# Kernel optimization log

Hardware: AMD Instinct MI355X
Metric: run time of the kernel (lower is better)

The kernel has to match this reference:

```python
import jax, jax.numpy as jnp
import numpy as np

P = 1_500_000
N_DEPTH = 6 * 118 * 16 * 44  # 498432 flattened depth bins
N_FEAT = 6 * 16 * 44         # 4224 flattened feature rows
TOTAL_BEV = 40000            # 200x200 BEV grid
C = 80


def setup_inputs() -> dict:
    key = jax.random.key(0)
    k1, k2, k3, k4, k5, k6, k7 = jax.random.split(key, 7)
    depth = jax.random.uniform(k1, (6, 118, 16, 44), dtype=jnp.float32)
    feat = jax.random.normal(k2, (6, 16, 44, C), dtype=jnp.float32)
    ranks_depth = jax.random.randint(k3, (P,), 0, N_DEPTH, dtype=jnp.int64)
    ranks_feat = jax.random.randint(k4, (P,), 0, N_FEAT, dtype=jnp.int64)
    ranks_bev = jnp.sort(jax.random.randint(k5, (P,), 0, TOTAL_BEV, dtype=jnp.int64))
    interval_starts = jnp.sort(jax.random.randint(k6, (TOTAL_BEV,), 0, P, dtype=jnp.int64))
    interval_lengths = jax.random.randint(k7, (TOTAL_BEV,), 0, 64, dtype=jnp.int64)
    return {
        "depth": depth,
        "feat": feat,
        "ranks_depth": ranks_depth,
        "ranks_feat": ranks_feat,
        "ranks_bev": ranks_bev,
        "interval_starts": interval_starts,
        "interval_lengths": interval_lengths,
        "total_bev": TOTAL_BEV,
    }


def reference(depth, feat, ranks_depth, ranks_feat, ranks_bev,
              interval_starts, interval_lengths, total_bev):
    # interval_starts / interval_lengths are unused (as in the torch source)
    channels = feat.shape[-1]
    feat_flat = feat.reshape(-1, channels).astype(jnp.float32)   # [N_feat, C]
    depth_flat = depth.reshape(-1).astype(jnp.float32)           # [N_depth]
    gathered_feat = feat_flat[ranks_feat]                        # [P, C]
    gathered_depth = depth_flat[ranks_depth][:, None]            # [P, 1]
    weighted_feat = gathered_feat * gathered_depth               # [P, C]
    out = jax.ops.segment_sum(weighted_feat, ranks_bev,
                              num_segments=int(total_bev))       # [total_bev, C]
    return out
```

## Files before the change

### kernel.cpp

```cpp
#include <hip/hip_runtime.h>
#include <hip/hip_fp16.h>


#define CHN 80

__global__ __launch_bounds__(256)
void prologue_kernel(const int* __restrict__ rb, int* __restrict__ seg,
                     const float* __restrict__ feat, __half* __restrict__ feat16,
                     int P, int total_bev, int nfeat) {
    const int gid = blockIdx.x * blockDim.x + threadIdx.x;
    if (gid < nfeat) feat16[gid] = __float2half(feat[gid]);

    const int i4 = gid * 4;
    if (i4 >= P) return;
    const int4 v = *reinterpret_cast<const int4*>(rb + i4);
    int prev = (i4 == 0) ? -1 : rb[i4 - 1];
    int cur;
    cur = v.x; for (int b = prev + 1; b <= cur; ++b) seg[b] = i4 + 0; prev = cur;
    cur = v.y; for (int b = prev + 1; b <= cur; ++b) seg[b] = i4 + 1; prev = cur;
    cur = v.z; for (int b = prev + 1; b <= cur; ++b) seg[b] = i4 + 2; prev = cur;
    cur = v.w; for (int b = prev + 1; b <= cur; ++b) seg[b] = i4 + 3; prev = cur;
    if (i4 + 4 >= P) {
        for (int b = prev + 1; b <= total_bev; ++b) seg[b] = P;
    }
}

__device__ __forceinline__ void acc8(float* a, const uint4& u, float d) {
    const __half2* h = reinterpret_cast<const __half2*>(&u);
#pragma unroll
    for (int k = 0; k < 4; ++k) {
        const float2 f = __half22float2(h[k]);
        a[2 * k]     += d * f.x;
        a[2 * k + 1] += d * f.y;
    }
}

__global__ __launch_bounds__(256)
void bev_pool_f16_kernel(const float* __restrict__ depth,
                         const __half* __restrict__ feat16,
                         const int* __restrict__ rd,
                         const int* __restrict__ rf,
                         const int* __restrict__ seg,
                         float* __restrict__ out,
                         int total_bev) {
    const int wave = threadIdx.x >> 6;
    const int lane = threadIdx.x & 63;
    const int bin = blockIdx.x * 4 + wave;
    if (bin >= total_bev) return;

    const int slot = lane >> 2;
    const int ll   = lane & 3;

    const int lo = seg[bin];
    const int hi = seg[bin + 1];

    float a[24];
#pragma unroll
    for (int k = 0; k < 24; ++k) a[k] = 0.f;

    int i = lo + slot;
    bool valid = i < hi;
    int di = 0, fi = 0;
    if (valid) { di = rd[i]; fi = rf[i]; }
    while (valid) {
        const int ni = i + 16;
        const bool nvalid = ni < hi;
        int ndi = 0, nfi = 0;
        if (nvalid) { ndi = rd[ni]; nfi = rf[ni]; }

        const float d = depth[di];
        const __half* row = feat16 + (size_t)fi * CHN;
        const uint4 u0 = *reinterpret_cast<const uint4*>(row + ll * 8);
        const uint4 u1 = *reinterpret_cast<const uint4*>(row + 32 + ll * 8);
        uint4 u2 = make_uint4(0u, 0u, 0u, 0u);
        if (ll < 2) u2 = *reinterpret_cast<const uint4*>(row + 64 + ll * 8);

        acc8(a + 0,  u0, d);
        acc8(a + 8,  u1, d);
        acc8(a + 16, u2, d);

        i = ni; di = ndi; fi = nfi; valid = nvalid;
    }

#pragma unroll
    for (int ofs = 4; ofs <= 32; ofs <<= 1) {
#pragma unroll
        for (int k = 0; k < 24; ++k) a[k] += __shfl_xor(a[k], ofs, 64);
    }

    float* orow = out + (size_t)bin * CHN;
    if (lane < 4) {
        const int b0 = lane * 8;
        *reinterpret_cast<float4*>(orow + b0)          = make_float4(a[0],  a[1],  a[2],  a[3]);
        *reinterpret_cast<float4*>(orow + b0 + 4)      = make_float4(a[4],  a[5],  a[6],  a[7]);
        *reinterpret_cast<float4*>(orow + 32 + b0)     = make_float4(a[8],  a[9],  a[10], a[11]);
        *reinterpret_cast<float4*>(orow + 36 + b0)     = make_float4(a[12], a[13], a[14], a[15]);
    } else if (lane < 6) {
        const int b2 = (lane - 4) * 8;
        *reinterpret_cast<float4*>(orow + 64 + b2)     = make_float4(a[16], a[17], a[18], a[19]);
        *reinterpret_cast<float4*>(orow + 68 + b2)     = make_float4(a[20], a[21], a[22], a[23]);
    }
}

__global__ __launch_bounds__(256)
void seg_starts_kernel(const int* __restrict__ rb, int* __restrict__ seg,
                       int P, int total_bev) {
    int q = blockIdx.x * blockDim.x + threadIdx.x;
    int i4 = q * 4;
    if (i4 >= P) return;
    const int4 v = *reinterpret_cast<const int4*>(rb + i4);
    int prev = (i4 == 0) ? -1 : rb[i4 - 1];
    int cur;
    cur = v.x; for (int b = prev + 1; b <= cur; ++b) seg[b] = i4 + 0; prev = cur;
    cur = v.y; for (int b = prev + 1; b <= cur; ++b) seg[b] = i4 + 1; prev = cur;
    cur = v.z; for (int b = prev + 1; b <= cur; ++b) seg[b] = i4 + 2; prev = cur;
    cur = v.w; for (int b = prev + 1; b <= cur; ++b) seg[b] = i4 + 3; prev = cur;
    if (i4 + 4 >= P) {
        for (int b = prev + 1; b <= total_bev; ++b) seg[b] = P;
    }
}

__global__ __launch_bounds__(256)
void bev_pool_f32_kernel(const float* __restrict__ depth,
                         const float* __restrict__ feat,
                         const int* __restrict__ rd,
                         const int* __restrict__ rf,
                         const int* __restrict__ seg,
                         float* __restrict__ out,
                         int total_bev) {
    const int wave = threadIdx.x >> 6;
    const int lane = threadIdx.x & 63;
    const int bin = blockIdx.x * 4 + wave;
    if (bin >= total_bev) return;
    const int slot = lane >> 2;
    const int ll   = lane & 3;
    const int lo = seg[bin];
    const int hi = seg[bin + 1];
    float4 a0 = make_float4(0.f, 0.f, 0.f, 0.f);
    float4 a1 = a0, a2 = a0, a3 = a0, a4 = a0;
    int i = lo + slot;
    bool valid = i < hi;
    int di = 0, fi = 0;
    if (valid) { di = rd[i]; fi = rf[i]; }
    while (valid) {
        const int ni = i + 16;
        const bool nvalid = ni < hi;
        int ndi = 0, nfi = 0;
        if (nvalid) { ndi = rd[ni]; nfi = rf[ni]; }
        const float d = depth[di];
        const float4* frow = reinterpret_cast<const float4*>(feat + (size_t)fi * CHN) + ll;
        const float4 f0 = frow[0], f1 = frow[4], f2 = frow[8], f3 = frow[12], f4 = frow[16];
        a0.x += d * f0.x; a0.y += d * f0.y; a0.z += d * f0.z; a0.w += d * f0.w;
        a1.x += d * f1.x; a1.y += d * f1.y; a1.z += d * f1.z; a1.w += d * f1.w;
        a2.x += d * f2.x; a2.y += d * f2.y; a2.z += d * f2.z; a2.w += d * f2.w;
        a3.x += d * f3.x; a3.y += d * f3.y; a3.z += d * f3.z; a3.w += d * f3.w;
        a4.x += d * f4.x; a4.y += d * f4.y; a4.z += d * f4.z; a4.w += d * f4.w;
        i = ni; di = ndi; fi = nfi; valid = nvalid;
    }
#pragma unroll
    for (int ofs = 4; ofs <= 32; ofs <<= 1) {
        a0.x += __shfl_xor(a0.x, ofs, 64); a0.y += __shfl_xor(a0.y, ofs, 64);
        a0.z += __shfl_xor(a0.z, ofs, 64); a0.w += __shfl_xor(a0.w, ofs, 64);
        a1.x += __shfl_xor(a1.x, ofs, 64); a1.y += __shfl_xor(a1.y, ofs, 64);
        a1.z += __shfl_xor(a1.z, ofs, 64); a1.w += __shfl_xor(a1.w, ofs, 64);
        a2.x += __shfl_xor(a2.x, ofs, 64); a2.y += __shfl_xor(a2.y, ofs, 64);
        a2.z += __shfl_xor(a2.z, ofs, 64); a2.w += __shfl_xor(a2.w, ofs, 64);
        a3.x += __shfl_xor(a3.x, ofs, 64); a3.y += __shfl_xor(a3.y, ofs, 64);
        a3.z += __shfl_xor(a3.z, ofs, 64); a3.w += __shfl_xor(a3.w, ofs, 64);
        a4.x += __shfl_xor(a4.x, ofs, 64); a4.y += __shfl_xor(a4.y, ofs, 64);
        a4.z += __shfl_xor(a4.z, ofs, 64); a4.w += __shfl_xor(a4.w, ofs, 64);
    }
    if (lane < 20) {
        const int j = lane >> 2;
        float4 w = a0;
        if (j == 1) w = a1;
        else if (j == 2) w = a2;
        else if (j == 3) w = a3;
        else if (j == 4) w = a4;
        *reinterpret_cast<float4*>(out + (size_t)bin * CHN + lane * 4) = w;
    }
}

extern "C" void kernel_launch(void* const* d_in, const int* in_sizes, int n_in,
                              void* d_out, int out_size, void* d_ws, size_t ws_size,
                              hipStream_t stream) {
    const float* depth = (const float*)d_in[0];
    const float* feat  = (const float*)d_in[1];
    const int*   rd    = (const int*)d_in[2];
    const int*   rf    = (const int*)d_in[3];
    const int*   rb    = (const int*)d_in[4];
    float* out = (float*)d_out;

    const int P = in_sizes[2];
    const int nfeat = in_sizes[1];
    const int total_bev = out_size / CHN;

    const size_t seg_bytes = ((size_t)(total_bev + 1) * 4 + 15) & ~(size_t)15;
    const size_t need = seg_bytes + (size_t)nfeat * 2;

    int* seg = (int*)d_ws;
    const int quads = (P + 3) / 4;
    const int quad_blocks = (quads + 255) / 256;

    if (ws_size >= need) {
        __half* feat16 = (__half*)((char*)d_ws + seg_bytes);
        const int cvt_blocks = (nfeat + 255) / 256;
        const int pro_blocks = quad_blocks > cvt_blocks ? quad_blocks : cvt_blocks;
        prologue_kernel<<<pro_blocks, 256, 0, stream>>>(rb, seg, feat, feat16,
                                                        P, total_bev, nfeat);
        bev_pool_f16_kernel<<<(total_bev + 3) / 4, 256, 0, stream>>>(
            depth, feat16, rd, rf, seg, out, total_bev);
    } else {
        seg_starts_kernel<<<quad_blocks, 256, 0, stream>>>(rb, seg, P, total_bev);
        bev_pool_f32_kernel<<<(total_bev + 3) / 4, 256, 0, stream>>>(
            depth, feat, rd, rf, seg, out, total_bev);
    }
}
```

Before: 127.2 us.

## Accumulate in packed half2 FMA, prefetch feature rows one step ahead, vectorize fp16 conversion

```diff
diff --git a/kernel.cpp b/kernel.cpp
--- a/kernel.cpp
+++ b/kernel.cpp
@@ -9,7 +9,15 @@
                      const float* __restrict__ feat, __half* __restrict__ feat16,
                      int P, int total_bev, int nfeat) {
     const int gid = blockIdx.x * blockDim.x + threadIdx.x;
-    if (gid < nfeat) feat16[gid] = __float2half(feat[gid]);
+    const int f4 = gid * 4;
+    if (f4 + 3 < nfeat) {
+        const float4 v = *reinterpret_cast<const float4*>(feat + f4);
+        __half2* dst = reinterpret_cast<__half2*>(feat16 + f4);
+        dst[0] = __floats2half2_rn(v.x, v.y);
+        dst[1] = __floats2half2_rn(v.z, v.w);
+    } else if (f4 < nfeat) {
+        for (int k = f4; k < nfeat; ++k) feat16[k] = __float2half(feat[k]);
+    }
 
     const int i4 = gid * 4;
     if (i4 >= P) return;
@@ -25,16 +33,6 @@
     }
 }
 
-__device__ __forceinline__ void acc8(float* a, const uint4& u, float d) {
-    const __half2* h = reinterpret_cast<const __half2*>(&u);
-#pragma unroll
-    for (int k = 0; k < 4; ++k) {
-        const float2 f = __half22float2(h[k]);
-        a[2 * k]     += d * f.x;
-        a[2 * k + 1] += d * f.y;
-    }
-}
-
 __global__ __launch_bounds__(256)
 void bev_pool_f16_kernel(const float* __restrict__ depth,
                          const __half* __restrict__ feat16,
@@ -54,34 +52,67 @@
     const int lo = seg[bin];
     const int hi = seg[bin + 1];
 
+    __half2 acc[12];
+#pragma unroll
+    for (int k = 0; k < 12; ++k) acc[k] = __half2half2(__float2half_rn(0.f));
+
+    int i0 = lo + slot;
+    bool v0 = i0 < hi;
+    int di0 = 0, fi0 = 0;
+    if (v0) { di0 = rd[i0]; fi0 = rf[i0]; }
+
+    int i1 = i0 + 16;
+    bool v1 = i1 < hi;
+    int di1 = 0, fi1 = 0;
+    if (v1) { di1 = rd[i1]; fi1 = rf[i1]; }
+
+    float d0 = 0.f;
+    uint4 u00 = make_uint4(0u, 0u, 0u, 0u), u01 = u00, u02 = u00;
+    if (v0) {
+        d0 = depth[di0];
+        const __half* row = feat16 + (size_t)fi0 * CHN;
+        u00 = *reinterpret_cast<const uint4*>(row + ll * 8);
+        u01 = *reinterpret_cast<const uint4*>(row + 32 + ll * 8);
+        if (ll < 2) u02 = *reinterpret_cast<const uint4*>(row + 64 + ll * 8);
+    }
+
+    while (v0) {
+        float d1 = 0.f;
+        uint4 u10 = make_uint4(0u, 0u, 0u, 0u), u11 = u10, u12 = u10;
+        if (v1) {
+            d1 = depth[di1];
+            const __half* row = feat16 + (size_t)fi1 * CHN;
+            u10 = *reinterpret_cast<const uint4*>(row + ll * 8);
+            u11 = *reinterpret_cast<const uint4*>(row + 32 + ll * 8);
+            if (ll < 2) u12 = *reinterpret_cast<const uint4*>(row + 64 + ll * 8);
+        }
+        const int i2 = i1 + 16;
+        const bool v2 = i2 < hi;
+        int di2 = 0, fi2 = 0;
+        if (v2) { di2 = rd[i2]; fi2 = rf[i2]; }
+
+        const __half2 dd = __half2half2(__float2half_rn(d0));
+        const __half2* h0 = reinterpret_cast<const __half2*>(&u00);
+        const __half2* h1 = reinterpret_cast<const __half2*>(&u01);
+        const __half2* h2 = reinterpret_cast<const __half2*>(&u02);
+#pragma unroll
+        for (int k = 0; k < 4; ++k) acc[k]     = __hfma2(dd, h0[k], acc[k]);
+#pragma unroll
+        for (int k = 0; k < 4; ++k) acc[4 + k] = __hfma2(dd, h1[k], acc[4 + k]);
+#pragma unroll
+        for (int k = 0; k < 4; ++k) acc[8 + k] = __hfma2(dd, h2[k], acc[8 + k]);
+
+        d0 = d1; u00 = u10; u01 = u11; u02 = u12;
+        v0 = v1; v1 = v2; i1 = i2; di1 = di2; fi1 = fi2;
+    }
+
     float a[24];
 #pragma unroll
-    for (int k = 0; k < 24; ++k) a[k] = 0.f;
-
-    int i = lo + slot;
-    bool valid = i < hi;
-    int di = 0, fi = 0;
-    if (valid) { di = rd[i]; fi = rf[i]; }
-    while (valid) {
-        const int ni = i + 16;
-        const bool nvalid = ni < hi;
-        int ndi = 0, nfi = 0;
-        if (nvalid) { ndi = rd[ni]; nfi = rf[ni]; }
-
-        const float d = depth[di];
-        const __half* row = feat16 + (size_t)fi * CHN;
-        const uint4 u0 = *reinterpret_cast<const uint4*>(row + ll * 8);
-        const uint4 u1 = *reinterpret_cast<const uint4*>(row + 32 + ll * 8);
-        uint4 u2 = make_uint4(0u, 0u, 0u, 0u);
-        if (ll < 2) u2 = *reinterpret_cast<const uint4*>(row + 64 + ll * 8);
-
-        acc8(a + 0,  u0, d);
-        acc8(a + 8,  u1, d);
-        acc8(a + 16, u2, d);
-
-        i = ni; di = ndi; fi = nfi; valid = nvalid;
-    }
-
+    for (int k = 0; k < 12; ++k) {
+        const float2 t = __half22float2(acc[k]);
+        a[2 * k]     = t.x;
+        a[2 * k + 1] = t.y;
+    }
 #pragma unroll
     for (int ofs = 4; ofs <= 32; ofs <<= 1) {
 #pragma unroll
@@ -91,14 +122,14 @@
     float* orow = out + (size_t)bin * CHN;
     if (lane < 4) {
         const int b0 = lane * 8;
-        *reinterpret_cast<float4*>(orow + b0)          = make_float4(a[0],  a[1],  a[2],  a[3]);
-        *reinterpret_cast<float4*>(orow + b0 + 4)      = make_float4(a[4],  a[5],  a[6],  a[7]);
-        *reinterpret_cast<float4*>(orow + 32 + b0)     = make_float4(a[8],  a[9],  a[10], a[11]);
-        *reinterpret_cast<float4*>(orow + 36 + b0)     = make_float4(a[12], a[13], a[14], a[15]);
+        *reinterpret_cast<float4*>(orow + b0)      = make_float4(a[0],  a[1],  a[2],  a[3]);
+        *reinterpret_cast<float4*>(orow + b0 + 4)  = make_float4(a[4],  a[5],  a[6],  a[7]);
+        *reinterpret_cast<float4*>(orow + 32 + b0) = make_float4(a[8],  a[9],  a[10], a[11]);
+        *reinterpret_cast<float4*>(orow + 36 + b0) = make_float4(a[12], a[13], a[14], a[15]);
     } else if (lane < 6) {
         const int b2 = (lane - 4) * 8;
-        *reinterpret_cast<float4*>(orow + 64 + b2)     = make_float4(a[16], a[17], a[18], a[19]);
-        *reinterpret_cast<float4*>(orow + 68 + b2)     = make_float4(a[20], a[21], a[22], a[23]);
+        *reinterpret_cast<float4*>(orow + 64 + b2) = make_float4(a[16], a[17], a[18], a[19]);
+        *reinterpret_cast<float4*>(orow + 68 + b2) = make_float4(a[20], a[21], a[22], a[23]);
     }
 }
 
@@ -204,7 +235,7 @@
 
     if (ws_size >= need) {
         __half* feat16 = (__half*)((char*)d_ws + seg_bytes);
-        const int cvt_blocks = (nfeat + 255) / 256;
+        const int cvt_blocks = ((nfeat + 3) / 4 + 255) / 256;
         const int pro_blocks = quad_blocks > cvt_blocks ? quad_blocks : cvt_blocks;
         prologue_kernel<<<pro_blocks, 256, 0, stream>>>(rb, seg, feat, feat16,
                                                         P, total_bev, nfeat);
```

After: 125.9 us. About the same (-1.0%).
